# Kernel optimization log

Measured on AMD Instinct MI355X. Metric: run time of the kernel, lower is better.

Reference implementation:

```python
import jax, jax.numpy as jnp
import numpy as np

N_NODES = 100000
N_EDGES = 1600000
D_IN = 128
D_OUT = 128


def setup_inputs() -> dict:
    key = jax.random.key(0)
    kx, ke, kw = jax.random.split(key, 3)
    x = jax.random.normal(kx, (N_NODES, D_IN), dtype=jnp.float32)
    edge_index = jax.random.randint(ke, (2, N_EDGES), 0, N_NODES, dtype=jnp.int32)
    W = jax.random.normal(kw, (D_IN, D_OUT), dtype=jnp.float32) / np.sqrt(D_IN)
    b = jnp.zeros((D_OUT,), dtype=jnp.float32)
    return {"x": x, "edge_index": edge_index, "W": W, "b": b}


def reference(x, edge_index, W, b):
    # PyG GCNConv: x' = D^{-1/2} (A + I) D^{-1/2} (x @ W) + b, then ReLU.
    n = x.shape[0]
    xw = x @ W  # linear transform first (as in GCNConv)
    # add self-loops
    loops = jnp.arange(n, dtype=edge_index.dtype)
    row = jnp.concatenate([edge_index[0], loops])  # source nodes
    col = jnp.concatenate([edge_index[1], loops])  # destination nodes
    # symmetric degree normalization (degree counted on destination, PyG-style)
    deg = jax.ops.segment_sum(jnp.ones_like(col, dtype=xw.dtype), col, num_segments=n)
    dinv = jnp.where(deg > 0, jax.lax.rsqrt(deg), 0.0)
    norm = dinv[row] * dinv[col]  # [E+N]
    # gather -> scale -> scatter-add
    msg = xw[row] * norm[:, None]  # [E+N, D_OUT]
    agg = jax.ops.segment_sum(msg, col, num_segments=n)  # [N, D_OUT]
    return jax.nn.relu(agg + b)
```

## Files before the change

kernel.cpp:

```cpp
#include <hip/hip_runtime.h>

#define DCH 128
#define T_PART 4096
#define B_MAX 512
#define CAPC 6144

typedef short bf16x8 __attribute__((ext_vector_type(8)));
typedef float f32x4 __attribute__((ext_vector_type(4)));

__device__ inline unsigned short f2bf(float f) {
    unsigned int u = __float_as_uint(f);
    unsigned int r = (u + 0x7fffu + ((u >> 16) & 1u)) >> 16;
    return (unsigned short)r;
}

__device__ inline void gload_lds16(const void* g, void* l) {
    __builtin_amdgcn_global_load_lds(
        (const __attribute__((address_space(1))) void*)g,
        (__attribute__((address_space(3))) void*)l, 16, 0, 0);
}

__global__ __launch_bounds__(256) void k_init(const float* __restrict__ W,
                                              unsigned short* __restrict__ Wf,
                                              int* __restrict__ gcount, int B) {
    int idx = blockIdx.x * 256 + threadIdx.x;
    if (idx < B) gcount[idx] = 0;
    int frag = blockIdx.x * 4 + (threadIdx.x >> 6);
    if (frag < 32) {
        int lane = threadIdx.x & 63;
        int nt = frag >> 2, ks = frag & 3;
        int nn = nt * 16 + (lane & 15);
        int k0 = ks * 32 + ((lane >> 4) * 8);
        unsigned short tmp[8];
#pragma unroll
        for (int j = 0; j < 8; ++j) tmp[j] = f2bf(W[(size_t)(k0 + j) * DCH + nn]);
        *(uint4*)&Wf[((size_t)frag * 64 + lane) * 8] = *(const uint4*)tmp;
    }
}

__global__ __launch_bounds__(512) void k_fused(const int* __restrict__ row,
                                               const int* __restrict__ col,
                                               unsigned int* __restrict__ coarse,
                                               int* __restrict__ gcount,
                                               const float* __restrict__ x,
                                               const unsigned short* __restrict__ Wf,
                                               unsigned short* __restrict__ y,
                                               int E, int B, int nPart, int n) {
    __shared__ uint4 smem4[4096];
    char* smem = (char*)smem4;

    int tid = threadIdx.x;
    int wv = tid >> 6, lane = tid & 63;

    if (blockIdx.x < nPart) {
        int* hist  = (int*)smem;
        int* basex = (int*)(smem + 2048);
        int* curx  = (int*)(smem + 4096);
        int* gb    = (int*)(smem + 6144);
        int* wsum  = (int*)(smem + 8192);
        unsigned int*   spack = (unsigned int*)(smem + 8320);
        unsigned short* sbuck = (unsigned short*)(smem + 24704);

        int base_e = blockIdx.x * T_PART;
        int tileCnt = min(T_PART, E - base_e);

        hist[tid] = 0;
        __syncthreads();

        int er[8], ec[8];
#pragma unroll
        for (int i = 0; i < 8; ++i) {
            int e = base_e + tid + i * 512;
            if (e < E) {
                er[i] = row[e];
                ec[i] = col[e];
                atomicAdd(&hist[ec[i] >> 8], 1);
            } else {
                er[i] = -1;
                ec[i] = 0;
            }
        }
        __syncthreads();

        int v = hist[tid];
        int x2 = v;
#pragma unroll
        for (int o = 1; o < 64; o <<= 1) {
            int t = __shfl_up(x2, o, 64);
            if (lane >= o) x2 += t;
        }
        if (lane == 63) wsum[wv] = x2;
        __syncthreads();
        int add = 0;
        for (int w = 0; w < wv; ++w) add += wsum[w];
        int excl = x2 - v + add;
        basex[tid] = excl;
        curx[tid] = excl;
        if (tid < B) gb[tid] = (v > 0) ? atomicAdd(&gcount[tid], v) : 0;
        else gb[tid] = 0;
        __syncthreads();

#pragma unroll
        for (int i = 0; i < 8; ++i) {
            if (er[i] >= 0) {
                int bb = ec[i] >> 8;
                int slot = atomicAdd(&curx[bb], 1);
                spack[slot] = ((unsigned int)er[i] << 8) | (unsigned int)(ec[i] & 255);
                sbuck[slot] = (unsigned short)bb;
            }
        }
        __syncthreads();

        for (int s = tid; s < tileCnt; s += 512) {
            int bb = sbuck[s];
            int dst = gb[bb] + (s - basex[bb]);
            if (dst < CAPC) coarse[(size_t)bb * CAPC + dst] = spack[s];
        }
    } else {
        int blockRow = (blockIdx.x - nPart) * 128;

#pragma unroll
        for (int t = 0; t < 8; ++t) {
            int off = t * 8192 + wv * 1024 + lane * 16;
            int r = off >> 9;
            int gr = blockRow + r;
            if (gr >= n) gr = n - 1;
            int colb = (off & 511) ^ ((r & 7) << 4);
            const char* src = (const char*)x + (size_t)gr * 512 + colb;
            char* dst = smem + t * 8192 + wv * 1024;
            gload_lds16(src, dst);
        }
        __syncthreads();

        f32x4 acc[8];
        f32x4 zero = {0.f, 0.f, 0.f, 0.f};
#pragma unroll
        for (int t = 0; t < 8; ++t) acc[t] = zero;

        const bf16x8* wfv = (const bf16x8*)Wf;
        int rowL = wv * 16 + (lane & 15);
        int q = lane >> 4;
        int swz = (rowL & 7) << 4;
#pragma unroll
        for (int ks = 0; ks < 4; ++ks) {
            int colb = ks * 128 + q * 32;
            float4 lo = *(const float4*)&smem[(rowL * 512 + colb) ^ swz];
            float4 hi = *(const float4*)&smem[(rowL * 512 + colb + 16) ^ swz];
            bf16x8 a;
            a[0] = (short)f2bf(lo.x); a[1] = (short)f2bf(lo.y);
            a[2] = (short)f2bf(lo.z); a[3] = (short)f2bf(lo.w);
            a[4] = (short)f2bf(hi.x); a[5] = (short)f2bf(hi.y);
            a[6] = (short)f2bf(hi.z); a[7] = (short)f2bf(hi.w);
#pragma unroll
            for (int nt = 0; nt < 8; ++nt) {
                bf16x8 bfr = wfv[(nt * 4 + ks) * 64 + lane];
                acc[nt] = __builtin_amdgcn_mfma_f32_16x16x32_bf16(a, bfr, acc[nt], 0, 0, 0);
            }
        }

        int rowBase = blockRow + wv * 16;
        int orow_base = rowBase + q * 4;
#pragma unroll
        for (int r = 0; r < 4; ++r) {
            int orow = orow_base + r;
            if (orow < n) {
#pragma unroll
                for (int nt = 0; nt < 8; ++nt) {
                    y[(size_t)orow * DCH + nt * 16 + (lane & 15)] = f2bf(acc[nt][r]);
                }
            }
        }
    }
}

__global__ __launch_bounds__(512) void k_csr(const unsigned int* __restrict__ coarse,
                                             const int* __restrict__ gcount,
                                             int* __restrict__ srow,
                                             int* __restrict__ off,
                                             float* __restrict__ dinvf,
                                             int n, int B) {
    __shared__ unsigned int ent[CAPC];
    __shared__ int h[256], cur[256];
    __shared__ int red1[8], red2[4];
    __shared__ int bbase_s;

    int b = blockIdx.x;
    int tid = threadIdx.x;
    int wv = tid >> 6, lane = tid & 63;

    int part = 0;
    for (int i = tid; i < b; i += 512) part += gcount[i];
#pragma unroll
    for (int o = 1; o < 64; o <<= 1) part += __shfl_xor(part, o, 64);
    if (lane == 0) red1[wv] = part;
    if (tid < 256) h[tid] = 0;
    __syncthreads();
    if (tid == 0) {
        int s = 0;
        for (int w = 0; w < 8; ++w) s += red1[w];
        bbase_s = s;
    }
    int cntb = min(gcount[b], CAPC);
    for (int s = tid; s < cntb; s += 512) ent[s] = coarse[(size_t)b * CAPC + s];
    __syncthreads();

    for (int s = tid; s < cntb; s += 512) atomicAdd(&h[ent[s] & 255], 1);
    __syncthreads();

    int x = 0, v = 0;
    if (tid < 256) {
        v = h[tid];
        x = v;
#pragma unroll
        for (int o = 1; o < 64; o <<= 1) {
            int t = __shfl_up(x, o, 64);
            if (lane >= o) x += t;
        }
        if (lane == 63) red2[wv] = x;
    }
    __syncthreads();
    if (tid < 256) {
        int add = 0;
        for (int w = 0; w < wv; ++w) add += red2[w];
        int excl = x - v + add;
        cur[tid] = excl;
        int node = (b << 8) + tid;
        if (node < n) {
            off[node] = bbase_s + excl;
            dinvf[node] = rsqrtf((float)(v + 1));
        }
    }
    __syncthreads();

    int bbase = bbase_s;
    for (int s = tid; s < cntb; s += 512) {
        unsigned int p = ent[s];
        int d = p & 255;
        int slot = atomicAdd(&cur[d], 1);
        srow[bbase + slot] = (int)(p >> 8);
    }
}

__global__ __launch_bounds__(256) void k_agg(const uint4* __restrict__ y4,
                                             const int* __restrict__ srow,
                                             const int* __restrict__ off,
                                             const float* __restrict__ dinv,
                                             const float* __restrict__ b,
                                             float* __restrict__ out, int n, int E) {
    int i = blockIdx.x * 4 + (threadIdx.x >> 6);
    if (i >= n) return;
    int lane = threadIdx.x & 63;
    int q = lane >> 4;
    int l16 = lane & 15;
    int s = off[i];
    int e = (i + 1 < n) ? off[i + 1] : E;
    float di = dinv[i];

    float acc[8];
#pragma unroll
    for (int k = 0; k < 8; ++k) acc[k] = 0.f;

    if (q == 0) {
        uint4 v = y4[(size_t)i * 16 + l16];
        unsigned int p[4] = {v.x, v.y, v.z, v.w};
#pragma unroll
        for (int t = 0; t < 4; ++t) {
            acc[2 * t]     = fmaf(di, __uint_as_float(p[t] << 16), acc[2 * t]);
            acc[2 * t + 1] = fmaf(di, __uint_as_float(p[t] & 0xffff0000u), acc[2 * t + 1]);
        }
    }

    int j = s;
    for (; j + 16 <= e; j += 16) {
        int s0 = srow[j + q];
        int s1 = srow[j + 4 + q];
        int s2 = srow[j + 8 + q];
        int s3 = srow[j + 12 + q];
        float d0 = dinv[s0], d1 = dinv[s1], d2 = dinv[s2], d3 = dinv[s3];
        uint4 v0 = y4[(size_t)s0 * 16 + l16];
        uint4 v1 = y4[(size_t)s1 * 16 + l16];
        uint4 v2 = y4[(size_t)s2 * 16 + l16];
        uint4 v3 = y4[(size_t)s3 * 16 + l16];
        unsigned int p0[4] = {v0.x, v0.y, v0.z, v0.w};
        unsigned int p1[4] = {v1.x, v1.y, v1.z, v1.w};
        unsigned int p2[4] = {v2.x, v2.y, v2.z, v2.w};
        unsigned int p3[4] = {v3.x, v3.y, v3.z, v3.w};
#pragma unroll
        for (int t = 0; t < 4; ++t) {
            acc[2 * t]     = fmaf(d0, __uint_as_float(p0[t] << 16), acc[2 * t]);
            acc[2 * t + 1] = fmaf(d0, __uint_as_float(p0[t] & 0xffff0000u), acc[2 * t + 1]);
            acc[2 * t]     = fmaf(d1, __uint_as_float(p1[t] << 16), acc[2 * t]);
            acc[2 * t + 1] = fmaf(d1, __uint_as_float(p1[t] & 0xffff0000u), acc[2 * t + 1]);
            acc[2 * t]     = fmaf(d2, __uint_as_float(p2[t] << 16), acc[2 * t]);
            acc[2 * t + 1] = fmaf(d2, __uint_as_float(p2[t] & 0xffff0000u), acc[2 * t + 1]);
            acc[2 * t]     = fmaf(d3, __uint_as_float(p3[t] << 16), acc[2 * t]);
            acc[2 * t + 1] = fmaf(d3, __uint_as_float(p3[t] & 0xffff0000u), acc[2 * t + 1]);
        }
    }
    for (; j + 8 <= e; j += 8) {
        int s0 = srow[j + q];
        int s1 = srow[j + 4 + q];
        float d0 = dinv[s0], d1 = dinv[s1];
        uint4 v0 = y4[(size_t)s0 * 16 + l16];
        uint4 v1 = y4[(size_t)s1 * 16 + l16];
        unsigned int p0[4] = {v0.x, v0.y, v0.z, v0.w};
        unsigned int p1[4] = {v1.x, v1.y, v1.z, v1.w};
#pragma unroll
        for (int t = 0; t < 4; ++t) {
            acc[2 * t]     = fmaf(d0, __uint_as_float(p0[t] << 16), acc[2 * t]);
            acc[2 * t + 1] = fmaf(d0, __uint_as_float(p0[t] & 0xffff0000u), acc[2 * t + 1]);
            acc[2 * t]     = fmaf(d1, __uint_as_float(p1[t] << 16), acc[2 * t]);
            acc[2 * t + 1] = fmaf(d1, __uint_as_float(p1[t] & 0xffff0000u), acc[2 * t + 1]);
        }
    }
    for (; j + 4 <= e; j += 4) {
        int s0 = srow[j + q];
        float d0 = dinv[s0];
        uint4 v0 = y4[(size_t)s0 * 16 + l16];
        unsigned int p0[4] = {v0.x, v0.y, v0.z, v0.w};
#pragma unroll
        for (int t = 0; t < 4; ++t) {
            acc[2 * t]     = fmaf(d0, __uint_as_float(p0[t] << 16), acc[2 * t]);
            acc[2 * t + 1] = fmaf(d0, __uint_as_float(p0[t] & 0xffff0000u), acc[2 * t + 1]);
        }
    }
    if (j + q < e) {
        int s0 = srow[j + q];
        float d0 = dinv[s0];
        uint4 v0 = y4[(size_t)s0 * 16 + l16];
        unsigned int p0[4] = {v0.x, v0.y, v0.z, v0.w};
#pragma unroll
        for (int t = 0; t < 4; ++t) {
            acc[2 * t]     = fmaf(d0, __uint_as_float(p0[t] << 16), acc[2 * t]);
            acc[2 * t + 1] = fmaf(d0, __uint_as_float(p0[t] & 0xffff0000u), acc[2 * t + 1]);
        }
    }

#pragma unroll
    for (int k = 0; k < 8; ++k) {
        acc[k] += __shfl_xor(acc[k], 16, 64);
        acc[k] += __shfl_xor(acc[k], 32, 64);
    }

    if (q == 0) {
        float sc = di;
        int c0 = l16 * 8;
        float4 b0 = *(const float4*)&b[c0];
        float4 b1 = *(const float4*)&b[c0 + 4];
        f32x4 o0, o1;
        o0[0] = fmaxf(fmaf(sc, acc[0], b0.x), 0.f);
        o0[1] = fmaxf(fmaf(sc, acc[1], b0.y), 0.f);
        o0[2] = fmaxf(fmaf(sc, acc[2], b0.z), 0.f);
        o0[3] = fmaxf(fmaf(sc, acc[3], b0.w), 0.f);
        o1[0] = fmaxf(fmaf(sc, acc[4], b1.x), 0.f);
        o1[1] = fmaxf(fmaf(sc, acc[5], b1.y), 0.f);
        o1[2] = fmaxf(fmaf(sc, acc[6], b1.z), 0.f);
        o1[3] = fmaxf(fmaf(sc, acc[7], b1.w), 0.f);
        f32x4* orow = (f32x4*)&out[(size_t)i * DCH + c0];
        __builtin_nontemporal_store(o0, &orow[0]);
        __builtin_nontemporal_store(o1, &orow[1]);
    }
}

extern "C" void kernel_launch(void* const* d_in, const int* in_sizes, int n_in,
                              void* d_out, int out_size, void* d_ws, size_t ws_size,
                              hipStream_t stream) {
    const float* x = (const float*)d_in[0];
    const int* ei  = (const int*)d_in[1];
    const float* W = (const float*)d_in[2];
    const float* b = (const float*)d_in[3];
    float* out = (float*)d_out;

    int n = in_sizes[0] / DCH;
    int E = in_sizes[1] / 2;
    const int* row = ei;
    const int* col = ei + E;

    int B = (n + 255) / 256;

    char* ws = (char*)d_ws;
    size_t o = 0;
    auto alloc = [&](size_t bytes) -> void* {
        o = (o + 255) & ~(size_t)255;
        void* p = ws + o;
        o += bytes;
        return p;
    };
    float* dinvf = (float*)alloc((size_t)n * 4);
    int* off     = (int*)alloc((size_t)(n + 1) * 4);
    int* gcount  = (int*)alloc((size_t)B * 4);
    int* srow    = (int*)alloc((size_t)E * 4);
    unsigned int* coarse = (unsigned int*)alloc((size_t)B * CAPC * 4);
    unsigned short* Wf = (unsigned short*)alloc((size_t)DCH * DCH * 2);
    unsigned short* y  = (unsigned short*)alloc((size_t)n * DCH * 2);

    int nt = (E + T_PART - 1) / T_PART;
    int gemmBlocks = (n + 127) / 128;
    k_init<<<8, 256, 0, stream>>>(W, Wf, gcount, B);
    k_fused<<<nt + gemmBlocks, 512, 0, stream>>>(row, col, coarse, gcount,
                                                 x, Wf, y, E, B, nt, n);
    k_csr<<<B, 512, 0, stream>>>(coarse, gcount, srow, off, dinvf, n, B);
    k_agg<<<(n + 3) / 4, 256, 0, stream>>>((const uint4*)y, srow, off, dinvf,
                                           b, out, n, E);
}
```

Baseline: 202.3 us.

## Regroup kernels: fuse W conversion into partition, GEMM into CSR build

Restructures the pipeline. The W-to-bf16 fragment conversion moves into extra blocks of the edge-partition kernel, and a memset replaces the init kernel for zeroing the bucket counters. The x@W GEMM moves out of the partition kernel into the CSR-build kernel, so the GEMM overlaps with CSR construction instead of with partitioning. GEMM tiles shrink to 64 rows and each pair of waves splits the output columns, halving shared memory per block. This drops one kernel launch and rebalances concurrent work, at the cost of smaller GEMM tiles that reload more W fragments.

```diff
diff --git a/kernel.cpp b/kernel.cpp
--- a/kernel.cpp
+++ b/kernel.cpp
@@ -20,125 +20,194 @@
         (__attribute__((address_space(3))) void*)l, 16, 0, 0);
 }
 
-__global__ __launch_bounds__(256) void k_init(const float* __restrict__ W,
-                                              unsigned short* __restrict__ Wf,
-                                              int* __restrict__ gcount, int B) {
-    int idx = blockIdx.x * 256 + threadIdx.x;
-    if (idx < B) gcount[idx] = 0;
-    int frag = blockIdx.x * 4 + (threadIdx.x >> 6);
-    if (frag < 32) {
-        int lane = threadIdx.x & 63;
-        int nt = frag >> 2, ks = frag & 3;
-        int nn = nt * 16 + (lane & 15);
-        int k0 = ks * 32 + ((lane >> 4) * 8);
-        unsigned short tmp[8];
-#pragma unroll
-        for (int j = 0; j < 8; ++j) tmp[j] = f2bf(W[(size_t)(k0 + j) * DCH + nn]);
-        *(uint4*)&Wf[((size_t)frag * 64 + lane) * 8] = *(const uint4*)tmp;
-    }
-}
-
-__global__ __launch_bounds__(512) void k_fused(const int* __restrict__ row,
-                                               const int* __restrict__ col,
-                                               unsigned int* __restrict__ coarse,
-                                               int* __restrict__ gcount,
-                                               const float* __restrict__ x,
-                                               const unsigned short* __restrict__ Wf,
-                                               unsigned short* __restrict__ y,
-                                               int E, int B, int nPart, int n) {
-    __shared__ uint4 smem4[4096];
-    char* smem = (char*)smem4;
-
+__global__ __launch_bounds__(512) void k_pg(const int* __restrict__ row,
+                                            const int* __restrict__ col,
+                                            unsigned int* __restrict__ coarse,
+                                            int* __restrict__ gcount,
+                                            const float* __restrict__ W,
+                                            unsigned short* __restrict__ Wf,
+                                            int E, int B, int nPart) {
     int tid = threadIdx.x;
     int wv = tid >> 6, lane = tid & 63;
 
-    if (blockIdx.x < nPart) {
-        int* hist  = (int*)smem;
-        int* basex = (int*)(smem + 2048);
-        int* curx  = (int*)(smem + 4096);
-        int* gb    = (int*)(smem + 6144);
-        int* wsum  = (int*)(smem + 8192);
-        unsigned int*   spack = (unsigned int*)(smem + 8320);
-        unsigned short* sbuck = (unsigned short*)(smem + 24704);
-
-        int base_e = blockIdx.x * T_PART;
-        int tileCnt = min(T_PART, E - base_e);
-
-        hist[tid] = 0;
-        __syncthreads();
-
-        int er[8], ec[8];
-#pragma unroll
-        for (int i = 0; i < 8; ++i) {
-            int e = base_e + tid + i * 512;
-            if (e < E) {
-                er[i] = row[e];
-                ec[i] = col[e];
-                atomicAdd(&hist[ec[i] >> 8], 1);
-            } else {
-                er[i] = -1;
-                ec[i] = 0;
+    if (blockIdx.x >= nPart) {
+        int frag = (blockIdx.x - nPart) * 8 + wv;
+        if (frag < 32) {
+            int nt = frag >> 2, ks = frag & 3;
+            int nn = nt * 16 + (lane & 15);
+            int k0 = ks * 32 + ((lane >> 4) * 8);
+            unsigned short tmp[8];
+#pragma unroll
+            for (int j = 0; j < 8; ++j) tmp[j] = f2bf(W[(size_t)(k0 + j) * DCH + nn]);
+            *(uint4*)&Wf[((size_t)frag * 64 + lane) * 8] = *(const uint4*)tmp;
+        }
+        return;
+    }
+
+    __shared__ unsigned int spack[T_PART];
+    __shared__ unsigned short sbuck[T_PART];
+    __shared__ int hist[B_MAX];
+    __shared__ int basex[B_MAX];
+    __shared__ int curx[B_MAX];
+    __shared__ int wsum[8];
+    int* gb = hist;
+
+    int base_e = blockIdx.x * T_PART;
+    int tileCnt = min(T_PART, E - base_e);
+
+    hist[tid] = 0;
+    __syncthreads();
+
+    int er[8], ec[8];
+#pragma unroll
+    for (int i = 0; i < 8; ++i) {
+        int e = base_e + tid + i * 512;
+        if (e < E) {
+            er[i] = row[e];
+            ec[i] = col[e];
+            atomicAdd(&hist[ec[i] >> 8], 1);
+        } else {
+            er[i] = -1;
+            ec[i] = 0;
+        }
+    }
+    __syncthreads();
+
+    int v = hist[tid];
+    int x2 = v;
+#pragma unroll
+    for (int o = 1; o < 64; o <<= 1) {
+        int t = __shfl_up(x2, o, 64);
+        if (lane >= o) x2 += t;
+    }
+    if (lane == 63) wsum[wv] = x2;
+    __syncthreads();
+    int add = 0;
+    for (int w = 0; w < wv; ++w) add += wsum[w];
+    int excl = x2 - v + add;
+    basex[tid] = excl;
+    curx[tid] = excl;
+    gb[tid] = (tid < B && v > 0) ? atomicAdd(&gcount[tid], v) : 0;
+    __syncthreads();
+
+#pragma unroll
+    for (int i = 0; i < 8; ++i) {
+        if (er[i] >= 0) {
+            int bb = ec[i] >> 8;
+            int slot = atomicAdd(&curx[bb], 1);
+            spack[slot] = ((unsigned int)er[i] << 8) | (unsigned int)(ec[i] & 255);
+            sbuck[slot] = (unsigned short)bb;
+        }
+    }
+    __syncthreads();
+
+    for (int s = tid; s < tileCnt; s += 512) {
+        int bb = sbuck[s];
+        int dst = gb[bb] + (s - basex[bb]);
+        if (dst < CAPC) coarse[(size_t)bb * CAPC + dst] = spack[s];
+    }
+}
+
+__global__ __launch_bounds__(512) void k_cg(const unsigned int* __restrict__ coarse,
+                                            const int* __restrict__ gcount,
+                                            int* __restrict__ srow,
+                                            int* __restrict__ off,
+                                            float* __restrict__ dinvf,
+                                            const float* __restrict__ x,
+                                            const unsigned short* __restrict__ Wf,
+                                            unsigned short* __restrict__ y,
+                                            int n, int B) {
+    __shared__ uint4 smem4[2048];
+    char* smem = (char*)smem4;
+
+    int tid = threadIdx.x;
+    int wv = tid >> 6, lane = tid & 63;
+
+    if (blockIdx.x < B) {
+        unsigned int* ent = (unsigned int*)smem;
+        int* h   = (int*)(smem + 24576);
+        int* cur = (int*)(smem + 25600);
+        int* red1 = (int*)(smem + 26624);
+        int* red2 = (int*)(smem + 26656);
+        int* bbase_p = (int*)(smem + 26672);
+
+        int b = blockIdx.x;
+
+        int part = 0;
+        for (int i = tid; i < b; i += 512) part += gcount[i];
+#pragma unroll
+        for (int o = 1; o < 64; o <<= 1) part += __shfl_xor(part, o, 64);
+        if (lane == 0) red1[wv] = part;
+        if (tid < 256) h[tid] = 0;
+        __syncthreads();
+        if (tid == 0) {
+            int s = 0;
+            for (int w = 0; w < 8; ++w) s += red1[w];
+            bbase_p[0] = s;
+        }
+        int cntb = min(gcount[b], CAPC);
+        for (int s = tid; s < cntb; s += 512) ent[s] = coarse[(size_t)b * CAPC + s];
+        __syncthreads();
+
+        for (int s = tid; s < cntb; s += 512) atomicAdd(&h[ent[s] & 255], 1);
+        __syncthreads();
+
+        int x2 = 0, v = 0;
+        if (tid < 256) {
+            v = h[tid];
+            x2 = v;
+#pragma unroll
+            for (int o = 1; o < 64; o <<= 1) {
+                int t = __shfl_up(x2, o, 64);
+                if (lane >= o) x2 += t;
             }
-        }
-        __syncthreads();
-
-        int v = hist[tid];
-        int x2 = v;
-#pragma unroll
-        for (int o = 1; o < 64; o <<= 1) {
-            int t = __shfl_up(x2, o, 64);
-            if (lane >= o) x2 += t;
-        }
-        if (lane == 63) wsum[wv] = x2;
-        __syncthreads();
-        int add = 0;
-        for (int w = 0; w < wv; ++w) add += wsum[w];
-        int excl = x2 - v + add;
-        basex[tid] = excl;
-        curx[tid] = excl;
-        if (tid < B) gb[tid] = (v > 0) ? atomicAdd(&gcount[tid], v) : 0;
-        else gb[tid] = 0;
-        __syncthreads();
-
-#pragma unroll
-        for (int i = 0; i < 8; ++i) {
-            if (er[i] >= 0) {
-                int bb = ec[i] >> 8;
-                int slot = atomicAdd(&curx[bb], 1);
-                spack[slot] = ((unsigned int)er[i] << 8) | (unsigned int)(ec[i] & 255);
-                sbuck[slot] = (unsigned short)bb;
+            if (lane == 63) red2[wv] = x2;
+        }
+        __syncthreads();
+        int bbase = bbase_p[0];
+        if (tid < 256) {
+            int add = 0;
+            for (int w = 0; w < wv; ++w) add += red2[w];
+            int excl = x2 - v + add;
+            cur[tid] = excl;
+            int node = (b << 8) + tid;
+            if (node < n) {
+                off[node] = bbase + excl;
+                dinvf[node] = rsqrtf((float)(v + 1));
             }
         }
         __syncthreads();
 
-        for (int s = tid; s < tileCnt; s += 512) {
-            int bb = sbuck[s];
-            int dst = gb[bb] + (s - basex[bb]);
-            if (dst < CAPC) coarse[(size_t)bb * CAPC + dst] = spack[s];
+        for (int s = tid; s < cntb; s += 512) {
+            unsigned int p = ent[s];
+            int d = p & 255;
+            int slot = atomicAdd(&cur[d], 1);
+            srow[bbase + slot] = (int)(p >> 8);
         }
     } else {
-        int blockRow = (blockIdx.x - nPart) * 128;
-
-#pragma unroll
-        for (int t = 0; t < 8; ++t) {
-            int off = t * 8192 + wv * 1024 + lane * 16;
-            int r = off >> 9;
+        int blockRow = (blockIdx.x - B) * 64;
+
+#pragma unroll
+        for (int t = 0; t < 4; ++t) {
+            int off2 = t * 8192 + wv * 1024 + lane * 16;
+            int r = off2 >> 9;
             int gr = blockRow + r;
             if (gr >= n) gr = n - 1;
-            int colb = (off & 511) ^ ((r & 7) << 4);
+            int colb = (off2 & 511) ^ ((r & 7) << 4);
             const char* src = (const char*)x + (size_t)gr * 512 + colb;
             char* dst = smem + t * 8192 + wv * 1024;
             gload_lds16(src, dst);
         }
         __syncthreads();
 
-        f32x4 acc[8];
+        f32x4 acc[4];
         f32x4 zero = {0.f, 0.f, 0.f, 0.f};
 #pragma unroll
-        for (int t = 0; t < 8; ++t) acc[t] = zero;
+        for (int t = 0; t < 4; ++t) acc[t] = zero;
 
         const bf16x8* wfv = (const bf16x8*)Wf;
-        int rowL = wv * 16 + (lane & 15);
+        int rowL = (wv >> 1) * 16 + (lane & 15);
+        int ntBase = (wv & 1) * 4;
         int q = lane >> 4;
         int swz = (rowL & 7) << 4;
 #pragma unroll
@@ -152,92 +221,26 @@
             a[4] = (short)f2bf(hi.x); a[5] = (short)f2bf(hi.y);
             a[6] = (short)f2bf(hi.z); a[7] = (short)f2bf(hi.w);
 #pragma unroll
-            for (int nt = 0; nt < 8; ++nt) {
+            for (int nt2 = 0; nt2 < 4; ++nt2) {
+                int nt = ntBase + nt2;
                 bf16x8 bfr = wfv[(nt * 4 + ks) * 64 + lane];
-                acc[nt] = __builtin_amdgcn_mfma_f32_16x16x32_bf16(a, bfr, acc[nt], 0, 0, 0);
+                acc[nt2] = __builtin_amdgcn_mfma_f32_16x16x32_bf16(a, bfr, acc[nt2], 0, 0, 0);
             }
         }
 
-        int rowBase = blockRow + wv * 16;
+        int rowBase = blockRow + (wv >> 1) * 16;
         int orow_base = rowBase + q * 4;
 #pragma unroll
         for (int r = 0; r < 4; ++r) {
             int orow = orow_base + r;
             if (orow < n) {
 #pragma unroll
-                for (int nt = 0; nt < 8; ++nt) {
-                    y[(size_t)orow * DCH + nt * 16 + (lane & 15)] = f2bf(acc[nt][r]);
+                for (int nt2 = 0; nt2 < 4; ++nt2) {
+                    int nt = ntBase + nt2;
+                    y[(size_t)orow * DCH + nt * 16 + (lane & 15)] = f2bf(acc[nt2][r]);
                 }
             }
         }
-    }
-}
-
-__global__ __launch_bounds__(512) void k_csr(const unsigned int* __restrict__ coarse,
-                                             const int* __restrict__ gcount,
-                                             int* __restrict__ srow,
-                                             int* __restrict__ off,
-                                             float* __restrict__ dinvf,
-                                             int n, int B) {
-    __shared__ unsigned int ent[CAPC];
-    __shared__ int h[256], cur[256];
-    __shared__ int red1[8], red2[4];
-    __shared__ int bbase_s;
-
-    int b = blockIdx.x;
-    int tid = threadIdx.x;
-    int wv = tid >> 6, lane = tid & 63;
-
-    int part = 0;
-    for (int i = tid; i < b; i += 512) part += gcount[i];
-#pragma unroll
-    for (int o = 1; o < 64; o <<= 1) part += __shfl_xor(part, o, 64);
-    if (lane == 0) red1[wv] = part;
-    if (tid < 256) h[tid] = 0;
-    __syncthreads();
-    if (tid == 0) {
-        int s = 0;
-        for (int w = 0; w < 8; ++w) s += red1[w];
-        bbase_s = s;
-    }
-    int cntb = min(gcount[b], CAPC);
-    for (int s = tid; s < cntb; s += 512) ent[s] = coarse[(size_t)b * CAPC + s];
-    __syncthreads();
-
-    for (int s = tid; s < cntb; s += 512) atomicAdd(&h[ent[s] & 255], 1);
-    __syncthreads();
-
-    int x = 0, v = 0;
-    if (tid < 256) {
-        v = h[tid];
-        x = v;
-#pragma unroll
-        for (int o = 1; o < 64; o <<= 1) {
-            int t = __shfl_up(x, o, 64);
-            if (lane >= o) x += t;
-        }
-        if (lane == 63) red2[wv] = x;
-    }
-    __syncthreads();
-    if (tid < 256) {
-        int add = 0;
-        for (int w = 0; w < wv; ++w) add += red2[w];
-        int excl = x - v + add;
-        cur[tid] = excl;
-        int node = (b << 8) + tid;
-        if (node < n) {
-            off[node] = bbase_s + excl;
-            dinvf[node] = rsqrtf((float)(v + 1));
-        }
-    }
-    __syncthreads();
-
-    int bbase = bbase_s;
-    for (int s = tid; s < cntb; s += 512) {
-        unsigned int p = ent[s];
-        int d = p & 255;
-        int slot = atomicAdd(&cur[d], 1);
-        srow[bbase + slot] = (int)(p >> 8);
     }
 }
 
@@ -395,11 +398,12 @@
     unsigned short* y  = (unsigned short*)alloc((size_t)n * DCH * 2);
 
     int nt = (E + T_PART - 1) / T_PART;
-    int gemmBlocks = (n + 127) / 128;
-    k_init<<<8, 256, 0, stream>>>(W, Wf, gcount, B);
-    k_fused<<<nt + gemmBlocks, 512, 0, stream>>>(row, col, coarse, gcount,
-                                                 x, Wf, y, E, B, nt, n);
-    k_csr<<<B, 512, 0, stream>>>(coarse, gcount, srow, off, dinvf, n, B);
+    int gemmBlocks = (n + 63) / 64;
+
+    hipMemsetAsync(gcount, 0, (size_t)B * 4, stream);
+    k_pg<<<nt + 4, 512, 0, stream>>>(row, col, coarse, gcount, W, Wf, E, B, nt);
+    k_cg<<<B + gemmBlocks, 512, 0, stream>>>(coarse, gcount, srow, off, dinvf,
+                                             x, Wf, y, n, B);
     k_agg<<<(n + 3) / 4, 256, 0, stream>>>((const uint4*)y, srow, off, dinvf,
                                            b, out, n, E);
 }
```

New measurement: 201.4 us. No clear change (-0.5%).
